# Kernel tuning notes

Hardware: AMD Instinct MI355X
Metric: run time of the kernel (lower is better)

Reference implementation:

```python
import jax, jax.numpy as jnp
import numpy as np

N_NODES = 50000


def gcn_conv(x, W, b, row, col, edge_weight):
    # PyG GCNConv (add_self_loops=False, normalize=True):
    # 1) linear transform, 2) symmetric normalization, 3) scatter-add aggregation
    h = x @ W  # [N, F_out]
    deg = jax.ops.segment_sum(edge_weight, col, num_segments=N_NODES)  # [N]
    dinv = jnp.where(deg > 0, jax.lax.rsqrt(deg), 0.0)
    norm = dinv[row] * edge_weight * dinv[col]  # [E]
    msgs = norm[:, None] * h[row]  # [E, F_out] gather
    out = jax.ops.segment_sum(msgs, col, num_segments=N_NODES)  # scatter-add
    return out + b


def setup_inputs() -> dict:
    key = jax.random.key(0)
    ks = jax.random.split(key, 7)
    E = 800000
    IN, HID, OUT = 256, 128, 16
    x = jax.random.normal(ks[0], (N_NODES, IN), dtype=jnp.float32)
    edge_index = jax.random.randint(ks[1], (2, E), 0, N_NODES, dtype=jnp.int64)
    edge_weight = jax.random.uniform(ks[2], (E,), dtype=jnp.float32)
    W1 = jax.random.normal(ks[3], (IN, HID), dtype=jnp.float32) * (1.0 / np.sqrt(IN))
    b1 = jnp.zeros((HID,), dtype=jnp.float32)
    W2 = jax.random.normal(ks[4], (HID, OUT), dtype=jnp.float32) * (1.0 / np.sqrt(HID))
    b2 = jnp.zeros((OUT,), dtype=jnp.float32)
    return {"x": x, "edge_index": edge_index, "edge_weight": edge_weight,
            "W1": W1, "b1": b1, "W2": W2, "b2": b2}


def reference(x, edge_index, edge_weight, W1, b1, W2, b2):
    row, col = edge_index[0], edge_index[1]
    h = jax.nn.relu(gcn_conv(x, W1, b1, row, col, edge_weight))
    # dropout is identity in eval mode
    h = gcn_conv(h, W2, b2, row, col, edge_weight)
    return jax.nn.log_softmax(h, axis=1)
```

## Files before the change

kernel.cpp:

```cpp
#include <hip/hip_runtime.h>
#include <hip/hip_bf16.h>

#define NN 50000
#define EE 800000
#define FIN 256
#define FH 128
#define FO 16
#define MAXDEG 64

using short8 = __attribute__((ext_vector_type(8))) short;
using f32x4  = __attribute__((ext_vector_type(4))) float;

__device__ __forceinline__ unsigned short f2b(float f) {
    unsigned int u = __float_as_uint(f);
    u += 0x7fffu + ((u >> 16) & 1u);
    return (unsigned short)(u >> 16);
}
__device__ __forceinline__ float b2f(unsigned short h) {
    return __uint_as_float(((unsigned int)h) << 16);
}

__global__ void prep_k(const unsigned int* __restrict__ ei, int* __restrict__ flag,
                       int* __restrict__ cursor,
                       const float* __restrict__ W1, const float* __restrict__ W2,
                       unsigned short* __restrict__ w1t, unsigned short* __restrict__ w2t) {
    int i = blockIdx.x * 256 + threadIdx.x;
    if (blockIdx.x == 0 && threadIdx.x < 64) {
        unsigned int v = (threadIdx.x < 32) ? ei[2 * threadIdx.x + 1] : 0u;
        unsigned long long ball = __ballot(v != 0u);
        if (threadIdx.x == 0) *flag = (ball == 0ull) ? 1 : 0;
    }
    if (i < NN) cursor[i] = 0;
    if (i < FH * FIN) {
        int n = i / FIN, k = i % FIN;
        w1t[i] = f2b(W1[k * FH + n]);
    }
    if (i < FO * FH) {
        int n = i / FH, k = i % FH;
        w2t[i] = f2b(W2[k * FO + n]);
    }
}

__device__ __forceinline__ void decode_edge(const void* ei, int int64flag, int e,
                                            int& r, int& c) {
    if (int64flag) {
        const long long* p = (const long long*)ei;
        r = (int)p[e]; c = (int)p[EE + e];
    } else {
        const int* p = (const int*)ei;
        r = p[e]; c = p[EE + e];
    }
    r = min(max(r, 0), NN - 1);
    c = min(max(c, 0), NN - 1);
}

__global__ void scatterpad_k(const void* __restrict__ ei, const float* __restrict__ ew,
                             const int* __restrict__ flag, int* __restrict__ cursor,
                             unsigned int* __restrict__ padj) {
    int e = blockIdx.x * 256 + threadIdx.x;
    if (e >= EE) return;
    int r, c;
    decode_edge(ei, *flag, e, r, c);
    float w = ew[e];
    int pos = atomicAdd(&cursor[c], 1);
    if (pos < MAXDEG)
        padj[c * MAXDEG + pos] = ((unsigned int)r << 16) | (unsigned int)f2b(w);
}

__global__ __launch_bounds__(256) void deg_k(const int* __restrict__ cursor,
                                             const unsigned int* __restrict__ padj,
                                             float* __restrict__ dinv) {
    const int n = blockIdx.x * 16 + (threadIdx.x >> 4);
    const int f = threadIdx.x & 15;
    const int cnt = min(cursor[n], MAXDEG);
    const unsigned int* base = padj + n * MAXDEG;
    float s = 0.f;
    for (int j = f; j < cnt; j += 16) s += b2f((unsigned short)(base[j] & 0xffff));
#pragma unroll
    for (int d = 1; d < 16; d <<= 1) s += __shfl_xor(s, d);
    if (f == 0) dinv[n] = (s > 0.f) ? rsqrtf(s) : 0.f;
}

__global__ __launch_bounds__(256) void gemm1_k(const float* __restrict__ X,
                                               const unsigned short* __restrict__ Bt,
                                               const float* __restrict__ dinv,
                                               unsigned short* __restrict__ C) {
    const int lane = threadIdx.x & 63;
    const int wave = threadIdx.x >> 6;
    const int m0 = blockIdx.x * 128 + wave * 32;
    const int lr = lane & 15;
    const int lk = (lane >> 4) * 8;
    f32x4 acc[2][8];
#pragma unroll
    for (int i = 0; i < 2; i++)
#pragma unroll
        for (int j = 0; j < 8; j++) acc[i][j] = (f32x4){0.f, 0.f, 0.f, 0.f};

    for (int k0 = 0; k0 < FIN; k0 += 32) {
        short8 a[2], b[8];
#pragma unroll
        for (int mi = 0; mi < 2; mi++) {
            int row = m0 + mi * 16 + lr;
            if (row >= NN) row = NN - 1;
            const float* ap = X + (size_t)row * FIN + k0 + lk;
            float4 v0 = *(const float4*)ap;
            float4 v1 = *(const float4*)(ap + 4);
            a[mi][0] = (short)f2b(v0.x); a[mi][1] = (short)f2b(v0.y);
            a[mi][2] = (short)f2b(v0.z); a[mi][3] = (short)f2b(v0.w);
            a[mi][4] = (short)f2b(v1.x); a[mi][5] = (short)f2b(v1.y);
            a[mi][6] = (short)f2b(v1.z); a[mi][7] = (short)f2b(v1.w);
        }
#pragma unroll
        for (int ni = 0; ni < 8; ni++)
            b[ni] = *(const short8*)(Bt + (ni * 16 + lr) * FIN + k0 + lk);
#pragma unroll
        for (int mi = 0; mi < 2; mi++)
#pragma unroll
            for (int ni = 0; ni < 8; ni++)
                acc[mi][ni] = __builtin_amdgcn_mfma_f32_16x16x32_bf16(
                    a[mi], b[ni], acc[mi][ni], 0, 0, 0);
    }
    const int r0 = (lane >> 4) * 4;
#pragma unroll
    for (int mi = 0; mi < 2; mi++)
#pragma unroll
        for (int r = 0; r < 4; r++) {
            int row = m0 + mi * 16 + r0 + r;
            if (row < NN) {
                float dv = dinv[row];
#pragma unroll
                for (int ni = 0; ni < 8; ni++)
                    C[(size_t)row * FH + ni * 16 + lr] = f2b(acc[mi][ni][r] * dv);
            }
        }
}

__global__ __launch_bounds__(256) void gemm2_k(const unsigned short* __restrict__ A,
                                               const unsigned short* __restrict__ Bt,
                                               const float* __restrict__ dinv,
                                               unsigned short* __restrict__ C) {
    const int lane = threadIdx.x & 63;
    const int wave = threadIdx.x >> 6;
    const int m0 = blockIdx.x * 128 + wave * 32;
    const int lr = lane & 15;
    const int lk = (lane >> 4) * 8;
    f32x4 acc[2];
    acc[0] = (f32x4){0.f, 0.f, 0.f, 0.f};
    acc[1] = (f32x4){0.f, 0.f, 0.f, 0.f};

    for (int k0 = 0; k0 < FH; k0 += 32) {
        short8 a[2], b;
#pragma unroll
        for (int mi = 0; mi < 2; mi++) {
            int row = m0 + mi * 16 + lr;
            if (row >= NN) row = NN - 1;
            a[mi] = *(const short8*)(A + (size_t)row * FH + k0 + lk);
        }
        b = *(const short8*)(Bt + lr * FH + k0 + lk);
#pragma unroll
        for (int mi = 0; mi < 2; mi++)
            acc[mi] = __builtin_amdgcn_mfma_f32_16x16x32_bf16(a[mi], b, acc[mi], 0, 0, 0);
    }
    const int r0 = (lane >> 4) * 4;
#pragma unroll
    for (int mi = 0; mi < 2; mi++)
#pragma unroll
        for (int r = 0; r < 4; r++) {
            int row = m0 + mi * 16 + r0 + r;
            if (row < NN) {
                float dv = dinv[row];
                C[(size_t)row * FO + lr] = f2b(acc[mi][r] * dv);
            }
        }
}

__global__ __launch_bounds__(256) void agg1_k(const int* __restrict__ cursor,
                                              const unsigned int* __restrict__ padj,
                                              const unsigned short* __restrict__ hlin,
                                              const float* __restrict__ dinv,
                                              const float* __restrict__ bias1,
                                              unsigned short* __restrict__ h1) {
    const int wid = blockIdx.x * 4 + (threadIdx.x >> 6);
    const int lane = threadIdx.x & 63;
    const int cnt = min(__builtin_amdgcn_readfirstlane(cursor[wid]), MAXDEG);
    const unsigned int* base = padj + wid * MAXDEG;
    const unsigned short* hp = hlin + 2 * lane;

    float s0[8], s1[8];
#pragma unroll
    for (int k = 0; k < 8; k++) { s0[k] = 0.f; s1[k] = 0.f; }

    int j = 0;
    for (; j + 8 <= cnt; j += 8) {
        unsigned int u[8], g[8];
#pragma unroll
        for (int k = 0; k < 8; k++) u[k] = base[j + k];
#pragma unroll
        for (int k = 0; k < 8; k++)
            g[k] = *(const unsigned int*)(hp + (size_t)(u[k] >> 16) * FH);
#pragma unroll
        for (int k = 0; k < 8; k++) {
            float n = b2f((unsigned short)(u[k] & 0xffff));
            s0[k] += n * b2f((unsigned short)(g[k] & 0xffff));
            s1[k] += n * b2f((unsigned short)(g[k] >> 16));
        }
    }
    for (; j + 4 <= cnt; j += 4) {
        unsigned int u[4], g[4];
#pragma unroll
        for (int k = 0; k < 4; k++) u[k] = base[j + k];
#pragma unroll
        for (int k = 0; k < 4; k++)
            g[k] = *(const unsigned int*)(hp + (size_t)(u[k] >> 16) * FH);
#pragma unroll
        for (int k = 0; k < 4; k++) {
            float n = b2f((unsigned short)(u[k] & 0xffff));
            s0[k] += n * b2f((unsigned short)(g[k] & 0xffff));
            s1[k] += n * b2f((unsigned short)(g[k] >> 16));
        }
    }
    for (; j < cnt; j++) {
        unsigned int u = base[j];
        unsigned int g = *(const unsigned int*)(hp + (size_t)(u >> 16) * FH);
        float n = b2f((unsigned short)(u & 0xffff));
        s0[0] += n * b2f((unsigned short)(g & 0xffff));
        s1[0] += n * b2f((unsigned short)(g >> 16));
    }
    float r0 = ((s0[0] + s0[1]) + (s0[2] + s0[3])) + ((s0[4] + s0[5]) + (s0[6] + s0[7]));
    float r1 = ((s1[0] + s1[1]) + (s1[2] + s1[3])) + ((s1[4] + s1[5]) + (s1[6] + s1[7]));
    float dc = dinv[wid];
    r0 = dc * r0 + bias1[2 * lane];
    r1 = dc * r1 + bias1[2 * lane + 1];
    unsigned int w = (unsigned int)f2b(fmaxf(r0, 0.f)) |
                     ((unsigned int)f2b(fmaxf(r1, 0.f)) << 16);
    *(unsigned int*)(h1 + (size_t)wid * FH + 2 * lane) = w;
}

__global__ __launch_bounds__(256) void agg2_k(const int* __restrict__ cursor,
                                              const unsigned int* __restrict__ padj,
                                              const unsigned short* __restrict__ h2lin,
                                              const float* __restrict__ dinv,
                                              const float* __restrict__ bias2,
                                              float* __restrict__ out) {
    const int g = threadIdx.x >> 4, f = threadIdx.x & 15;
    const int n = blockIdx.x * 16 + g;
    const int cnt = min(cursor[n], MAXDEG);
    const unsigned int* base = padj + n * MAXDEG;
    float s[8];
#pragma unroll
    for (int k = 0; k < 8; k++) s[k] = 0.f;

    int j = 0;
    for (; j + 8 <= cnt; j += 8) {
        unsigned int u[8];
        float v[8];
#pragma unroll
        for (int k = 0; k < 8; k++) u[k] = base[j + k];
#pragma unroll
        for (int k = 0; k < 8; k++) v[k] = b2f(h2lin[(size_t)(u[k] >> 16) * FO + f]);
#pragma unroll
        for (int k = 0; k < 8; k++) s[k] += b2f((unsigned short)(u[k] & 0xffff)) * v[k];
    }
    for (; j + 4 <= cnt; j += 4) {
        unsigned int u[4];
        float v[4];
#pragma unroll
        for (int k = 0; k < 4; k++) u[k] = base[j + k];
#pragma unroll
        for (int k = 0; k < 4; k++) v[k] = b2f(h2lin[(size_t)(u[k] >> 16) * FO + f]);
#pragma unroll
        for (int k = 0; k < 4; k++) s[k] += b2f((unsigned short)(u[k] & 0xffff)) * v[k];
    }
    for (; j < cnt; j++) {
        unsigned int u = base[j];
        s[0] += b2f((unsigned short)(u & 0xffff)) * b2f(h2lin[(size_t)(u >> 16) * FO + f]);
    }
    float acc = ((s[0] + s[1]) + (s[2] + s[3])) + ((s[4] + s[5]) + (s[6] + s[7]));
    acc = dinv[n] * acc + bias2[f];
    float m = acc;
#pragma unroll
    for (int d = 1; d < 16; d <<= 1) m = fmaxf(m, __shfl_xor(m, d));
    float ex = expf(acc - m);
    float sum = ex;
#pragma unroll
    for (int d = 1; d < 16; d <<= 1) sum += __shfl_xor(sum, d);
    out[(size_t)n * FO + f] = acc - m - logf(sum);
}

extern "C" void kernel_launch(void* const* d_in, const int* in_sizes, int n_in,
                              void* d_out, int out_size, void* d_ws, size_t ws_size,
                              hipStream_t stream) {
    const float* x  = (const float*)d_in[0];
    const void*  ei = d_in[1];
    const float* ew = (const float*)d_in[2];
    const float* W1 = (const float*)d_in[3];
    const float* b1 = (const float*)d_in[4];
    const float* W2 = (const float*)d_in[5];
    const float* b2 = (const float*)d_in[6];
    float* out = (float*)d_out;

    char* base = (char*)d_ws;
    size_t off = 0;
    auto alloc = [&](size_t bytes) {
        void* p = base + off;
        off += (bytes + 255) & ~(size_t)255;
        return p;
    };
    int*          flag   = (int*)alloc(4);
    int*          cursor = (int*)alloc(NN * 4);
    float*        dinv   = (float*)alloc(NN * 4);
    unsigned int* padj   = (unsigned int*)alloc((size_t)NN * MAXDEG * 4);
    unsigned short* w1t   = (unsigned short*)alloc(FH * FIN * 2);
    unsigned short* w2t   = (unsigned short*)alloc(FO * FH * 2);
    unsigned short* h1lin = (unsigned short*)alloc((size_t)NN * FH * 2);
    unsigned short* h1    = (unsigned short*)alloc((size_t)NN * FH * 2);
    unsigned short* h2lin = (unsigned short*)alloc((size_t)NN * FO * 2);
    (void)ws_size; (void)n_in; (void)in_sizes; (void)out_size;

    const int NB = (NN + 255) / 256;

    prep_k<<<NB, 256, 0, stream>>>((const unsigned int*)ei, flag, cursor, W1, W2, w1t, w2t);
    scatterpad_k<<<EE / 256, 256, 0, stream>>>(ei, ew, flag, cursor, padj);
    deg_k<<<NN / 16, 256, 0, stream>>>(cursor, padj, dinv);

    gemm1_k<<<(NN + 127) / 128, 256, 0, stream>>>(x, w1t, dinv, h1lin);
    agg1_k<<<NN / 4, 256, 0, stream>>>(cursor, padj, h1lin, dinv, b1, h1);
    gemm2_k<<<(NN + 127) / 128, 256, 0, stream>>>(h1, w2t, dinv, h2lin);
    agg2_k<<<NN / 16, 256, 0, stream>>>(cursor, padj, h2lin, dinv, b2, out);
}
```

Before: 217.9 us.

## Build padded adjacency via two-pass bucket partition with shared-memory staging

Replaces per-edge global atomics into a node-indexed padded adjacency with a two-pass scheme. Edges are first partitioned into 256-node buckets using shared-memory histograms and one global atomic per bucket per block. Each bucket is then assembled in shared memory, where degree normalisation is also computed, and written out coalesced. This removes the scattered global atomics and the separate degree kernel. In exchange it uses 64KB of LDS per block, reuses the h1lin buffer as scratch, and relies on a fixed per-bucket capacity that could truncate edges for skewed graphs.

```diff
diff --git a/kernel.cpp b/kernel.cpp
--- a/kernel.cpp
+++ b/kernel.cpp
@@ -7,6 +7,10 @@
 #define FH 128
 #define FO 16
 #define MAXDEG 64
+#define NBKT 196
+#define BCAP 5120
+#define EPB 2048
+#define PB ((EE + EPB - 1) / EPB)
 
 using short8 = __attribute__((ext_vector_type(8))) short;
 using f32x4  = __attribute__((ext_vector_type(4))) float;
@@ -21,7 +25,7 @@
 }
 
 __global__ void prep_k(const unsigned int* __restrict__ ei, int* __restrict__ flag,
-                       int* __restrict__ cursor,
+                       int* __restrict__ bcur,
                        const float* __restrict__ W1, const float* __restrict__ W2,
                        unsigned short* __restrict__ w1t, unsigned short* __restrict__ w2t) {
     int i = blockIdx.x * 256 + threadIdx.x;
@@ -30,7 +34,7 @@
         unsigned long long ball = __ballot(v != 0u);
         if (threadIdx.x == 0) *flag = (ball == 0ull) ? 1 : 0;
     }
-    if (i < NN) cursor[i] = 0;
+    if (i < NBKT * 16) bcur[i] = 0;
     if (i < FH * FIN) {
         int n = i / FIN, k = i % FIN;
         w1t[i] = f2b(W1[k * FH + n]);
@@ -54,31 +58,84 @@
     c = min(max(c, 0), NN - 1);
 }
 
-__global__ void scatterpad_k(const void* __restrict__ ei, const float* __restrict__ ew,
-                             const int* __restrict__ flag, int* __restrict__ cursor,
-                             unsigned int* __restrict__ padj) {
-    int e = blockIdx.x * 256 + threadIdx.x;
-    if (e >= EE) return;
-    int r, c;
-    decode_edge(ei, *flag, e, r, c);
-    float w = ew[e];
-    int pos = atomicAdd(&cursor[c], 1);
-    if (pos < MAXDEG)
-        padj[c * MAXDEG + pos] = ((unsigned int)r << 16) | (unsigned int)f2b(w);
-}
-
-__global__ __launch_bounds__(256) void deg_k(const int* __restrict__ cursor,
-                                             const unsigned int* __restrict__ padj,
-                                             float* __restrict__ dinv) {
-    const int n = blockIdx.x * 16 + (threadIdx.x >> 4);
-    const int f = threadIdx.x & 15;
-    const int cnt = min(cursor[n], MAXDEG);
-    const unsigned int* base = padj + n * MAXDEG;
-    float s = 0.f;
-    for (int j = f; j < cnt; j += 16) s += b2f((unsigned short)(base[j] & 0xffff));
-#pragma unroll
-    for (int d = 1; d < 16; d <<= 1) s += __shfl_xor(s, d);
-    if (f == 0) dinv[n] = (s > 0.f) ? rsqrtf(s) : 0.f;
+__global__ __launch_bounds__(256) void part_k(const void* __restrict__ ei,
+                                              const float* __restrict__ ew,
+                                              const int* __restrict__ flag,
+                                              int* __restrict__ bcur,
+                                              uint2* __restrict__ part) {
+    __shared__ int hist[NBKT];
+    __shared__ int lcur[NBKT];
+    const int t = threadIdx.x;
+    const int e0 = blockIdx.x * EPB;
+    for (int i = t; i < NBKT; i += 256) hist[i] = 0;
+    __syncthreads();
+
+    const int fl = *flag;
+    int r[8], c[8], bk[8];
+    float w[8];
+#pragma unroll
+    for (int k = 0; k < 8; k++) {
+        int e = e0 + k * 256 + t;
+        if (e < EE) {
+            decode_edge(ei, fl, e, r[k], c[k]);
+            w[k] = ew[e];
+            bk[k] = c[k] >> 8;
+            atomicAdd(&hist[bk[k]], 1);
+        } else bk[k] = -1;
+    }
+    __syncthreads();
+    if (t < NBKT) {
+        int h = hist[t];
+        lcur[t] = (h > 0) ? atomicAdd(&bcur[t * 16], h) : 0;
+    }
+    __syncthreads();
+#pragma unroll
+    for (int k = 0; k < 8; k++) {
+        if (bk[k] >= 0) {
+            int pos = atomicAdd(&lcur[bk[k]], 1);
+            if (pos < BCAP)
+                part[(size_t)bk[k] * BCAP + pos] =
+                    make_uint2(((unsigned int)r[k] << 16) | (unsigned int)c[k],
+                               __float_as_uint(w[k]));
+        }
+    }
+}
+
+__global__ __launch_bounds__(256) void build_k(const int* __restrict__ bcur,
+                                               const uint2* __restrict__ part,
+                                               unsigned int* __restrict__ padj,
+                                               int* __restrict__ cursor,
+                                               float* __restrict__ dinv) {
+    __shared__ int cnt[256];
+    __shared__ unsigned int staged[256 * MAXDEG];
+    const int b = blockIdx.x, t = threadIdx.x;
+    cnt[t] = 0;
+    __syncthreads();
+
+    const int ecnt = min(bcur[b * 16], BCAP);
+    const uint2* src = part + (size_t)b * BCAP;
+    for (int j = t; j < ecnt; j += 256) {
+        uint2 e = src[j];
+        int cl = (int)(e.x & 0xffff) - (b << 8);
+        int pos = atomicAdd(&cnt[cl], 1);
+        if (pos < MAXDEG)
+            staged[cl * MAXDEG + pos] =
+                (e.x & 0xffff0000u) | (unsigned int)f2b(__uint_as_float(e.y));
+    }
+    __syncthreads();
+
+    const int n = (b << 8) + t;
+    if (n < NN) {
+        int cc = min(cnt[t], MAXDEG);
+        cursor[n] = cc;
+        float s = 0.f;
+        for (int j = 0; j < cc; j++)
+            s += b2f((unsigned short)(staged[t * MAXDEG + j] & 0xffff));
+        dinv[n] = (s > 0.f) ? rsqrtf(s) : 0.f;
+    }
+    const size_t obase = (size_t)b * 256 * MAXDEG;
+    for (int idx = t; idx < 256 * MAXDEG; idx += 256)
+        padj[obase + idx] = staged[idx];
 }
 
 __global__ __launch_bounds__(256) void gemm1_k(const float* __restrict__ X,
@@ -183,7 +240,7 @@
     const int wid = blockIdx.x * 4 + (threadIdx.x >> 6);
     const int lane = threadIdx.x & 63;
     const int cnt = min(__builtin_amdgcn_readfirstlane(cursor[wid]), MAXDEG);
-    const unsigned int* base = padj + wid * MAXDEG;
+    const unsigned int* base = padj + (size_t)wid * MAXDEG;
     const unsigned short* hp = hlin + 2 * lane;
 
     float s0[8], s1[8];
@@ -245,7 +302,7 @@
     const int g = threadIdx.x >> 4, f = threadIdx.x & 15;
     const int n = blockIdx.x * 16 + g;
     const int cnt = min(cursor[n], MAXDEG);
-    const unsigned int* base = padj + n * MAXDEG;
+    const unsigned int* base = padj + (size_t)n * MAXDEG;
     float s[8];
 #pragma unroll
     for (int k = 0; k < 8; k++) s[k] = 0.f;
@@ -307,21 +364,23 @@
         return p;
     };
     int*          flag   = (int*)alloc(4);
+    int*          bcur   = (int*)alloc((size_t)NBKT * 16 * 4);
     int*          cursor = (int*)alloc(NN * 4);
     float*        dinv   = (float*)alloc(NN * 4);
-    unsigned int* padj   = (unsigned int*)alloc((size_t)NN * MAXDEG * 4);
+    unsigned int* padj   = (unsigned int*)alloc((size_t)NBKT * 256 * MAXDEG * 4);
     unsigned short* w1t   = (unsigned short*)alloc(FH * FIN * 2);
     unsigned short* w2t   = (unsigned short*)alloc(FO * FH * 2);
     unsigned short* h1lin = (unsigned short*)alloc((size_t)NN * FH * 2);
     unsigned short* h1    = (unsigned short*)alloc((size_t)NN * FH * 2);
     unsigned short* h2lin = (unsigned short*)alloc((size_t)NN * FO * 2);
+    uint2* part = (uint2*)h1lin;
     (void)ws_size; (void)n_in; (void)in_sizes; (void)out_size;
 
     const int NB = (NN + 255) / 256;
 
-    prep_k<<<NB, 256, 0, stream>>>((const unsigned int*)ei, flag, cursor, W1, W2, w1t, w2t);
-    scatterpad_k<<<EE / 256, 256, 0, stream>>>(ei, ew, flag, cursor, padj);
-    deg_k<<<NN / 16, 256, 0, stream>>>(cursor, padj, dinv);
+    prep_k<<<NB, 256, 0, stream>>>((const unsigned int*)ei, flag, bcur, W1, W2, w1t, w2t);
+    part_k<<<PB, 256, 0, stream>>>(ei, ew, flag, bcur, part);
+    build_k<<<NBKT, 256, 0, stream>>>(bcur, part, padj, cursor, dinv);
 
     gemm1_k<<<(NN + 127) / 128, 256, 0, stream>>>(x, w1t, dinv, h1lin);
     agg1_k<<<NN / 4, 256, 0, stream>>>(cursor, padj, h1lin, dinv, b1, h1);
```

Result: faster. 193.4 us (-11.2%).
